# Kernel tuning notes

Hardware: AMD Instinct MI355X
Metric: run time of the kernel (lower is better)

Reference implementation:

```python
import jax, jax.numpy as jnp
import numpy as np

B, N, D, H, FF = 2, 2048, 768, 12, 3072
HD = D // H
RADIUS = 2.0
COORD_DIM = 3
LN_EPS = 1e-5


def _layernorm(x, g, b):
    m = jnp.mean(x, axis=-1, keepdims=True)
    v = jnp.mean((x - m) ** 2, axis=-1, keepdims=True)
    return (x - m) * jax.lax.rsqrt(v + LN_EPS) * g + b


def setup_inputs() -> dict:
    key = jax.random.key(0)
    ks = jax.random.split(key, 16)
    s = 0.02
    return {
        "x": jax.random.normal(ks[0], (B, N, D), jnp.float32),
        "coords": jax.random.uniform(ks[1], (B, N, COORD_DIM), jnp.float32) * 10.0,
        "w_qkv": jax.random.normal(ks[2], (D, 3 * D), jnp.float32) * s,
        "b_qkv": jnp.zeros((3 * D,), jnp.float32),
        "w_out": jax.random.normal(ks[3], (D, D), jnp.float32) * s,
        "b_out": jnp.zeros((D,), jnp.float32),
        "w_ff1": jax.random.normal(ks[4], (D, FF), jnp.float32) * s,
        "b_ff1": jnp.zeros((FF,), jnp.float32),
        "w_ff2": jax.random.normal(ks[5], (FF, D), jnp.float32) * s,
        "b_ff2": jnp.zeros((D,), jnp.float32),
        "g1": jnp.ones((D,), jnp.float32),
        "beta1": jnp.zeros((D,), jnp.float32),
        "g2": jnp.ones((D,), jnp.float32),
        "beta2": jnp.zeros((D,), jnp.float32),
    }


def reference(x, coords, w_qkv, b_qkv, w_out, b_out, w_ff1, b_ff1,
              w_ff2, b_ff2, g1, beta1, g2, beta2):
    # --- attention sub-block ---
    residual = x
    xn = _layernorm(x, g1, beta1)
    qkv = xn @ w_qkv + b_qkv                       # [B,N,3D]
    qkv = qkv.reshape(B, N, 3, H, HD)
    q, k, v = qkv[:, :, 0], qkv[:, :, 1], qkv[:, :, 2]   # [B,N,H,HD]

    # geometric radius mask: attend only to tokens within Euclidean RADIUS
    d2 = jnp.sum((coords[:, :, None, :] - coords[:, None, :, :]) ** 2, axis=-1)  # [B,N,N]
    mask = d2 <= RADIUS * RADIUS                   # self-distance 0 -> always true

    scores = jnp.einsum("bqhd,bkhd->bhqk", q, k) / jnp.sqrt(jnp.float32(HD))
    scores = jnp.where(mask[:, None, :, :], scores, jnp.float32(-1e9))
    attn = jax.nn.softmax(scores, axis=-1)
    attn_out = jnp.einsum("bhqk,bkhd->bqhd", attn, v).reshape(B, N, D)
    attn_out = attn_out @ w_out + b_out            # dropout=0 (eval)
    x = residual + attn_out

    # --- FFN sub-block ---
    residual = x
    xn = _layernorm(x, g2, beta2)
    h = jax.nn.gelu(xn @ w_ff1 + b_ff1, approximate=False)
    ff_out = h @ w_ff2 + b_ff2
    return residual + ff_out
```

## Files before the change

### kernel.cpp

```cpp
#include <hip/hip_runtime.h>
#include <hip/hip_bf16.h>

typedef unsigned short ushort_t;
typedef __attribute__((ext_vector_type(4))) float f32x4;
typedef __attribute__((ext_vector_type(8))) short s16x8;

#define DEV static __device__ __forceinline__

constexpr int Bb = 2, Nn = 2048, Dd = 768, Hh = 12, FFf = 3072;
constexpr int MTOK = Bb * Nn;
constexpr int QKVN = 3 * Dd;

DEV unsigned short f2bf(float f) {
    union { float f; unsigned int i; } x; x.f = f;
    unsigned int r = x.i + 0x7FFFu + ((x.i >> 16) & 1u);
    return (unsigned short)(r >> 16);
}

DEV void gload16(const void* g, void* l) {
    __builtin_amdgcn_global_load_lds(
        (const __attribute__((address_space(1))) void*)g,
        (__attribute__((address_space(3))) void*)l, 16, 0, 0);
}

DEV int xcd_swz(int lin, int n) {
    return (lin & 7) * (n >> 3) + (lin >> 3);
}

DEV float gelu_fast(float x) {
    float u = x * (0.7978845608f + 0.0356774081f * x * x);
    float e = __builtin_amdgcn_exp2f(2.885390082f * u);
    float th = 1.f - 2.f / (e + 1.f);
    return 0.5f * x * (1.f + th);
}

__global__ void k_transpose_all(const float* __restrict__ w_qkv, const float* __restrict__ w_out,
                                const float* __restrict__ w_ff1, const float* __restrict__ w_ff2,
                                unsigned short* __restrict__ o_qkv, unsigned short* __restrict__ o_out,
                                unsigned short* __restrict__ o_ff1, unsigned short* __restrict__ o_ff2) {
    __shared__ float t[32][33];
    int id = blockIdx.x;
    const float* in; unsigned short* out; int K, N, tid;
    if (id < 1728)      { in = w_qkv; out = o_qkv; K = 768;  N = 2304; tid = id; }
    else if (id < 2304) { in = w_out; out = o_out; K = 768;  N = 768;  tid = id - 1728; }
    else if (id < 4608) { in = w_ff1; out = o_ff1; K = 768;  N = 3072; tid = id - 2304; }
    else                { in = w_ff2; out = o_ff2; K = 3072; N = 768;  tid = id - 4608; }
    int nbx = N >> 5;
    int bx = (tid % nbx) * 32, by = (tid / nbx) * 32;
    int tx = threadIdx.x, ty = threadIdx.y;
#pragma unroll
    for (int i = 0; i < 4; i++)
        t[ty + 8 * i][tx] = in[(size_t)(by + ty + 8 * i) * N + bx + tx];
    __syncthreads();
#pragma unroll
    for (int i = 0; i < 4; i++)
        out[(size_t)(bx + ty + 8 * i) * K + by + tx] = f2bf(t[tx][ty + 8 * i]);
}

DEV int cell3(float x, float y, float z) {
    int cx = (int)(x * 0.5f); cx = cx > 4 ? 4 : cx;
    int cy = (int)(y * 0.5f); cy = cy > 4 ? 4 : cy;
    int cz = (int)(z * 0.5f); cz = cz > 4 ? 4 : cz;
    return (cz * 5 + cy) * 5 + cx;
}

__global__ __launch_bounds__(256) void k_sort(const float* __restrict__ coords,
                                              int* __restrict__ s2o,
                                              float4* __restrict__ c4s) {
    int b = blockIdx.y;
    int i = blockIdx.x * 4 + (threadIdx.x >> 6);
    int lane = threadIdx.x & 63;
    const float* cb = coords + (size_t)b * Nn * 3;
    float cix = cb[3 * i], ciy = cb[3 * i + 1], ciz = cb[3 * i + 2];
    int celli = cell3(cix, ciy, ciz);
    int pos = 0;
    for (int it = 0; it < Nn / 64; it++) {
        int j = it * 64 + lane;
        int cj = cell3(cb[3 * j], cb[3 * j + 1], cb[3 * j + 2]);
        bool before = (cj < celli) || (cj == celli && j < i);
        pos += __popcll(__ballot(before));
    }
    if (lane == 0) {
        s2o[b * Nn + pos] = i;
        c4s[b * Nn + pos] = make_float4(cix, ciy, ciz, 0.f);
    }
}

__global__ __launch_bounds__(256) void k_mask(const float4* __restrict__ c4s,
                                              unsigned long long* __restrict__ mb) {
    int qt = blockIdx.x, ks = blockIdx.y, b = blockIdx.z;
    __shared__ float4 ck[256];
    int t = threadIdx.x;
    ck[t] = c4s[b * Nn + ks * 256 + t];
    __syncthreads();
    int r = t >> 2, c = t & 3;
    int q = qt * 64 + r;
    float4 cq = c4s[b * Nn + q];
    unsigned long long w = 0;
#pragma unroll 8
    for (int j = 0; j < 64; j++) {
        float4 k4 = ck[c * 64 + j];
        float dx = __fsub_rn(cq.x, k4.x);
        float dy = __fsub_rn(cq.y, k4.y);
        float dz = __fsub_rn(cq.z, k4.z);
        float d2 = __fadd_rn(__fadd_rn(__fmul_rn(dx, dx), __fmul_rn(dy, dy)),
                             __fmul_rn(dz, dz));
        if (d2 <= 4.0f) w |= 1ull << j;
    }
    mb[((size_t)(b * Nn + q) << 5) + ks * 4 + c] = w;
}

__global__ __launch_bounds__(64) void k_tiles(const unsigned long long* __restrict__ mb,
                                              int* __restrict__ tl) {
    int q64 = blockIdx.x, b = blockIdx.y;
    int lane = threadIdx.x;
    unsigned long long v = 0;
    if (lane < 32) {
        const unsigned long long* base = mb + ((size_t)(b * Nn + q64 * 64) << 5) + lane;
        for (int r = 0; r < 64; r++) v |= base[(size_t)r << 5];
    }
    unsigned long long nz = __ballot(v != 0);
    int idx = __popcll(nz & ((1ull << lane) - 1));
    int* o = tl + (b * 32 + q64) * 33;
    if (v != 0) o[1 + idx] = lane;
    if (lane == 0) o[0] = __popcll(nz);
}

__global__ __launch_bounds__(128) void k_gatherK(const unsigned short* __restrict__ qkv,
                                                 const int* __restrict__ s2o,
                                                 unsigned short* __restrict__ Ksort) {
    int ns = blockIdx.x & (Nn - 1);
    int b = blockIdx.x >> 11;
    int t = threadIdx.x;
    int orig = s2o[b * Nn + ns];
    const s16x8* src = (const s16x8*)(qkv + ((size_t)b * Nn + orig) * QKVN + Dd);
    s16x8* dst = (s16x8*)(Ksort + ((size_t)b * Nn + ns) * Dd);
    if (t < 96) dst[t] = src[t];
}

__global__ __launch_bounds__(256) void k_vt(const unsigned short* __restrict__ qkv,
                                            const int* __restrict__ s2o,
                                            unsigned short* __restrict__ VtT) {
    __shared__ unsigned short Ld[64][72];
    int ns0 = blockIdx.x * 64;
    int bh = blockIdx.y;
    int b = bh / Hh, h = bh % Hh;
    int t = threadIdx.x;
#pragma unroll
    for (int i = 0; i < 2; i++) {
        int item = t + 256 * i;
        int row = item >> 3, ch = (item & 7) * 8;
        int orig = s2o[b * Nn + ns0 + row];
        *(s16x8*)&Ld[row][ch] =
            *(const s16x8*)(qkv + ((size_t)b * Nn + orig) * QKVN + 2 * Dd + h * 64 + ch);
    }
    __syncthreads();
    int vd = (t >> 5) * 8, vkp = (t & 31) * 2;
#pragma unroll
    for (int j = 0; j < 8; j++) {
        unsigned int pack = (unsigned int)Ld[vkp][vd + j] |
                            ((unsigned int)Ld[vkp + 1][vd + j] << 16);
        *(unsigned int*)((char*)VtT +
                         (((size_t)bh * 64 + vd + j) * Nn + ns0 + vkp) * 2) = pack;
    }
}

DEV float wred_sum(float v) {
#pragma unroll
    for (int o = 32; o; o >>= 1) v += __shfl_down(v, o, 64);
    return v;
}

__global__ __launch_bounds__(256) void k_ln(const float* __restrict__ x,
                                            const float* __restrict__ g,
                                            const float* __restrict__ be,
                                            unsigned short* __restrict__ out) {
    int row = blockIdx.x;
    const float* xr = x + (size_t)row * Dd;
    int t = threadIdx.x;
    float v0 = xr[t], v1 = xr[t + 256], v2 = xr[t + 512];
    float s = v0 + v1 + v2;
    float sq = v0 * v0 + v1 * v1 + v2 * v2;
    __shared__ float r1[4], r2[4];
    float ws = wred_sum(s), wq = wred_sum(sq);
    int wid = t >> 6, lane = t & 63;
    if (lane == 0) { r1[wid] = ws; r2[wid] = wq; }
    __syncthreads();
    s = r1[0] + r1[1] + r1[2] + r1[3];
    sq = r2[0] + r2[1] + r2[2] + r2[3];
    float mean = s * (1.f / Dd);
    float var = sq * (1.f / Dd) - mean * mean;
    float rs = rsqrtf(var + 1e-5f);
    unsigned short* orow = out + (size_t)row * Dd;
    orow[t]       = f2bf((v0 - mean) * rs * g[t]       + be[t]);
    orow[t + 256] = f2bf((v1 - mean) * rs * g[t + 256] + be[t + 256]);
    orow[t + 512] = f2bf((v2 - mean) * rs * g[t + 512] + be[t + 512]);
}

#define GEMM_PIPE_LOOP(NT)                                                              \
    stage(0, 0);                                                                        \
    if ((NT) > 1) stage(1, 1);                                                          \
    for (int t = 0; t < (NT); t++) {                                                    \
        int cur = t % 3;                                                                \
        if (t + 2 < (NT)) {                                                             \
            stage((t + 2) % 3, t + 2);                                                  \
            asm volatile("s_waitcnt vmcnt(8)" ::: "memory");                            \
        } else if (t + 1 < (NT)) {                                                      \
            asm volatile("s_waitcnt vmcnt(4)" ::: "memory");                            \
        } else {                                                                        \
            asm volatile("s_waitcnt vmcnt(0)" ::: "memory");                            \
        }                                                                               \
        __builtin_amdgcn_sched_barrier(0);                                              \
        __builtin_amdgcn_s_barrier();                                                   \
        const unsigned short* Ab = As[cur];                                             \
        const unsigned short* Bbp = Bs[cur];                                            \
        s16x8 af[4], bfr[4];                                                            \
        _Pragma("unroll")                                                               \
        for (int i = 0; i < 4; i++) {                                                   \
            af[i]  = *(const s16x8*)&Ab[(wr * 64 + i * 16 + lr) * 32 + lg * 8];         \
            bfr[i] = *(const s16x8*)&Bbp[(wc * 64 + i * 16 + lr) * 32 + lg * 8];        \
        }                                                                               \
        __builtin_amdgcn_s_setprio(1);                                                  \
        _Pragma("unroll")                                                               \
        for (int mi = 0; mi < 4; mi++)                                                  \
            _Pragma("unroll")                                                           \
            for (int ni = 0; ni < 4; ni++)                                              \
                acc[mi][ni] = __builtin_amdgcn_mfma_f32_16x16x32_bf16(                  \
                    af[mi], bfr[ni], acc[mi][ni], 0, 0, 0);                             \
        __builtin_amdgcn_s_setprio(0);                                                  \
        __builtin_amdgcn_s_barrier();                                                   \
    }

template <int EPI>
__global__ __launch_bounds__(256) void k_gemm(const unsigned short* __restrict__ A,
                                              const unsigned short* __restrict__ Bt,
                                              const float* __restrict__ bias,
                                              const float* __restrict__ res,
                                              void* __restrict__ outp,
                                              int M, int N, int K) {
    constexpr int BM = 128, BN = 128, BK = 32;
    __shared__ unsigned short As[3][BM * BK];
    __shared__ unsigned short Bs[3][BN * BK];
    int NB = N >> 7;
    int id = xcd_swz(blockIdx.x, gridDim.x);
    int m0 = (id / NB) * BM, n0 = (id % NB) * BN;
    int t = threadIdx.x;
    int wid = t >> 6, lane = t & 63;
    int wr = wid >> 1, wc = wid & 1;
    int lg = lane >> 4, lr = lane & 15;
    f32x4 acc[4][4] = {};

    int srow = wid * 32 + (lane >> 2);
    int scol = (lane & 3) * 8;
    const unsigned short* Ag = A + (size_t)(m0 + srow) * K + scol;
    const unsigned short* Bg = Bt + (size_t)(n0 + srow) * K + scol;

    auto stage = [&](int buf, int kt) {
        int k0 = kt * BK;
        char* Al = (char*)As[buf] + wid * 2048;
        char* Bl = (char*)Bs[buf] + wid * 2048;
        gload16(Ag + k0, Al);
        gload16(Ag + k0 + (size_t)16 * K, Al + 1024);
        gload16(Bg + k0, Bl);
        gload16(Bg + k0 + (size_t)16 * K, Bl + 1024);
    };
    int nt = K / BK;
    GEMM_PIPE_LOOP(nt)

    int mrow = m0 + wr * 64;
    int ncol = n0 + wc * 64;
#pragma unroll
    for (int mi = 0; mi < 4; mi++) {
#pragma unroll
        for (int ni = 0; ni < 4; ni++) {
            int nn = ncol + ni * 16 + lr;
            float bs = bias[nn];
#pragma unroll
            for (int r = 0; r < 4; r++) {
                int mm = mrow + mi * 16 + lg * 4 + r;
                float v = acc[mi][ni][r] + bs;
                if (EPI == 1) {
                    ((unsigned short*)outp)[(size_t)mm * N + nn] = f2bf(gelu_fast(v));
                } else if (EPI == 2) {
                    v += res[(size_t)mm * N + nn];
                    ((float*)outp)[(size_t)mm * N + nn] = v;
                } else {
                    ((unsigned short*)outp)[(size_t)mm * N + nn] = f2bf(v);
                }
            }
        }
    }
}

template <int SPLIT>
__global__ __launch_bounds__(256) void k_gemm_sk(const unsigned short* __restrict__ A,
                                                 const unsigned short* __restrict__ Bt,
                                                 float* __restrict__ part,
                                                 int M, int N, int K) {
    constexpr int BM = 128, BN = 128, BK = 32;
    __shared__ unsigned short As[3][BM * BK];
    __shared__ unsigned short Bs[3][BN * BK];
    int NB = N >> 7, MB = M >> 7;
    int id = xcd_swz(blockIdx.x, gridDim.x);
    int nb = id % NB;
    int mbk = (id / NB) % MB;
    int kz = id / (NB * MB);
    int m0 = mbk * BM, n0 = nb * BN;
    int Kc = K / SPLIT, kb = kz * (Kc / BK);
    int t = threadIdx.x;
    int wid = t >> 6, lane = t & 63;
    int wr = wid >> 1, wc = wid & 1;
    int lg = lane >> 4, lr = lane & 15;
    f32x4 acc[4][4] = {};

    int srow = wid * 32 + (lane >> 2);
    int scol = (lane & 3) * 8;
    const unsigned short* Ag = A + (size_t)(m0 + srow) * K + scol;
    const unsigned short* Bg = Bt + (size_t)(n0 + srow) * K + scol;

    auto stage = [&](int buf, int kt) {
        int k0 = (kb + kt) * BK;
        char* Al = (char*)As[buf] + wid * 2048;
        char* Bl = (char*)Bs[buf] + wid * 2048;
        gload16(Ag + k0, Al);
        gload16(Ag + k0 + (size_t)16 * K, Al + 1024);
        gload16(Bg + k0, Bl);
        gload16(Bg + k0 + (size_t)16 * K, Bl + 1024);
    };
    int nt = Kc / BK;
    GEMM_PIPE_LOOP(nt)

    float* po = part + (size_t)kz * M * N;
    int mrow = m0 + wr * 64;
    int ncol = n0 + wc * 64;
#pragma unroll
    for (int mi = 0; mi < 4; mi++)
#pragma unroll
        for (int ni = 0; ni < 4; ni++) {
            int nn = ncol + ni * 16 + lr;
#pragma unroll
            for (int r = 0; r < 4; r++) {
                int mm = mrow + mi * 16 + lg * 4 + r;
                po[(size_t)mm * N + nn] = acc[mi][ni][r];
            }
        }
}

__global__ __launch_bounds__(256) void k_reduce2(const float* __restrict__ part,
                                                 const float* __restrict__ bias,
                                                 const float* __restrict__ res,
                                                 float* __restrict__ out,
                                                 int MN, int N) {
    int i = (blockIdx.x * 256 + threadIdx.x) * 4;
    f32x4 a = *(const f32x4*)(part + i);
    f32x4 bq = *(const f32x4*)(part + (size_t)MN + i);
    f32x4 r = *(const f32x4*)(res + i);
    f32x4 bs = *(const f32x4*)(bias + (i % N));
    f32x4 o;
#pragma unroll
    for (int j = 0; j < 4; j++) o[j] = a[j] + bq[j] + bs[j] + r[j];
    *(f32x4*)(out + i) = o;
}

constexpr float SC2 = 0.125f * 1.44269504088896340736f;
constexpr float PMASK = -3.0e38f;
constexpr float MINIT = -1.0e30f;

__global__ __launch_bounds__(256) void k_attn(const unsigned short* __restrict__ qkv,
                                              const unsigned short* __restrict__ Ksort,
                                              const unsigned short* __restrict__ VtT,
                                              const int* __restrict__ s2o,
                                              const uint2* __restrict__ mb,
                                              const int* __restrict__ tl,
                                              unsigned short* __restrict__ out) {
    int lin = blockIdx.x;
    int id = (lin & 7) * 96 + (lin >> 3);
    int q64 = id & 31;
    int hb = id >> 5;
    int h = hb % Hh, b = hb / Hh;
    int bh = b * Hh + h;

    __shared__ __align__(16) char sm[2 * 16384 + 4 * 2048];

    int t = threadIdx.x, wid = t >> 6, lane = t & 63;
    int lg = lane >> 4, lr = lane & 15;
    int sw = lr & 7;
    int qbase = q64 * 64 + wid * 16;

    int oq = s2o[b * Nn + qbase + lr];
    const unsigned short* Qb = qkv + ((size_t)b * Nn + oq) * QKVN + h * 64;
    s16x8 qf0 = *(const s16x8*)(Qb + lg * 8);
    s16x8 qf1 = *(const s16x8*)(Qb + 32 + lg * 8);

    const uint2* mrow = mb + ((size_t)(b * Nn + qbase + lr) << 5);
    const int* tle = tl + (b * 32 + q64) * 33;
    int tlv = (lane < 33) ? tle[lane] : 0;
    int cnt = __shfl(tlv, 0, 64);

    int srow = lane >> 3, sch = lane & 7;
    int krow = wid * 8 + srow;
    int kx = sch ^ (krow & 7);
    const unsigned short* Kg0 = Ksort + ((size_t)b * Nn + krow) * Dd + h * 64 + kx * 8;
    const unsigned short* Vg0 = VtT + ((size_t)bh * 64 + krow) * Nn + kx * 8;
    char* pw = sm + 32768 + wid * 2048 + lr * 128;

    float m2 = MINIT, l_run = 0.f;
    f32x4 oacc[4] = {};

    int tid0 = __shfl(tlv, 1, 64);
    uint2 Mw = mrow[tid0];
    {
        char* Kl = sm + wid * 1024;
        gload16(Kg0 + (size_t)(tid0 * 64) * Dd, Kl);
        gload16(Kg0 + (size_t)(tid0 * 64 + 32) * Dd, Kl + 4096);
        char* Vl = sm + 8192 + wid * 1024;
        gload16(Vg0 + tid0 * 64, Vl);
        gload16(Vg0 + tid0 * 64 + 32 * (size_t)Nn, Vl + 4096);
    }
    __syncthreads();

    for (int ti = 0; ti < cnt; ti++) {
        int cur = ti & 1;
        uint2 MwN;
        if (ti + 1 < cnt) {
            int tidn = __shfl(tlv, 2 + ti, 64);
            char* Kl = sm + (cur ^ 1) * 16384 + wid * 1024;
            gload16(Kg0 + (size_t)(tidn * 64) * Dd, Kl);
            gload16(Kg0 + (size_t)(tidn * 64 + 32) * Dd, Kl + 4096);
            char* Vl = sm + (cur ^ 1) * 16384 + 8192 + wid * 1024;
            gload16(Vg0 + tidn * 64, Vl);
            gload16(Vg0 + tidn * 64 + 32 * (size_t)Nn, Vl + 4096);
            MwN = mrow[tidn];
        }

        if (__any((Mw.x | Mw.y) != 0)) {
            const char* Kbuf = sm + cur * 16384;
            const char* Vbuf = Kbuf + 8192;

            __builtin_amdgcn_s_setprio(1);
            f32x4 st[4];
#pragma unroll
            for (int s = 0; s < 4; s++) {
                const char* kr = Kbuf + (s * 16 + lr) * 128;
                s16x8 kf0 = *(const s16x8*)(kr + ((lg ^ sw) << 4));
                s16x8 kf1 = *(const s16x8*)(kr + (((4 + lg) ^ sw) << 4));
                f32x4 z = {};
                z = __builtin_amdgcn_mfma_f32_16x16x32_bf16(kf0, qf0, z, 0, 0, 0);
                st[s] = __builtin_amdgcn_mfma_f32_16x16x32_bf16(kf1, qf1, z, 0, 0, 0);
            }
            __builtin_amdgcn_s_setprio(0);

            float p[4][4];
            float mt = PMASK;
#pragma unroll
            for (int s = 0; s < 4; s++) {
                unsigned int wsel = (s < 2) ? Mw.x : Mw.y;
#pragma unroll
                for (int r = 0; r < 4; r++) {
                    float sv = st[s][r] * SC2;
                    unsigned int bit = (wsel >> ((s & 1) * 16 + lg * 4 + r)) & 1u;
                    p[s][r] = bit ? sv : PMASK;
                    mt = fmaxf(mt, p[s][r]);
                }
            }
            mt = fmaxf(mt, __shfl_xor(mt, 16, 64));
            mt = fmaxf(mt, __shfl_xor(mt, 32, 64));

            if (!__all(mt <= m2 + 11.5416f)) {
                float mn2 = fmaxf(m2, mt);
                float fac = __builtin_amdgcn_exp2f(m2 - mn2);
                l_run *= fac;
                m2 = mn2;
                float fr[4];
#pragma unroll
                for (int r = 0; r < 4; r++) fr[r] = __shfl(fac, (lane & 48) + lg * 4 + r, 64);
#pragma unroll
                for (int dt = 0; dt < 4; dt++)
#pragma unroll
                    for (int r = 0; r < 4; r++) oacc[dt][r] *= fr[r];
            }

            float lt = 0.f;
#pragma unroll
            for (int s = 0; s < 4; s++)
#pragma unroll
                for (int r = 0; r < 4; r++) {
                    p[s][r] = __builtin_amdgcn_exp2f(p[s][r] - m2);
                    lt += p[s][r];
                }
            lt += __shfl_xor(lt, 16, 64);
            lt += __shfl_xor(lt, 32, 64);
            l_run += lt;

#pragma unroll
            for (int s = 0; s < 4; s++) {
                unsigned int lo = (unsigned int)f2bf(p[s][0]) | ((unsigned int)f2bf(p[s][1]) << 16);
                unsigned int hi = (unsigned int)f2bf(p[s][2]) | ((unsigned int)f2bf(p[s][3]) << 16);
                unsigned long long u = (unsigned long long)lo | ((unsigned long long)hi << 32);
                int chunk = (s * 2 + (lg >> 1)) ^ sw;
                *(unsigned long long*)(pw + (chunk << 4) + (lg & 1) * 8) = u;
            }

            __builtin_amdgcn_s_setprio(1);
#pragma unroll
            for (int c = 0; c < 2; c++) {
                s16x8 pf = *(const s16x8*)(pw + (((c * 4 + lg) ^ sw) << 4));
#pragma unroll
                for (int dt = 0; dt < 4; dt++) {
                    const char* vr = Vbuf + (dt * 16 + lr) * 128;
                    s16x8 vf = *(const s16x8*)(vr + (((c * 4 + lg) ^ sw) << 4));
                    oacc[dt] = __builtin_amdgcn_mfma_f32_16x16x32_bf16(pf, vf, oacc[dt], 0, 0, 0);
                }
            }
            __builtin_amdgcn_s_setprio(0);
        }

        __syncthreads();
        Mw = MwN;
    }

    float lr4[4];
    int orow[4];
#pragma unroll
    for (int r = 0; r < 4; r++) {
        lr4[r] = __shfl(l_run, (lane & 48) + lg * 4 + r, 64);
        orow[r] = s2o[b * Nn + qbase + lg * 4 + r];
    }
#pragma unroll
    for (int dt = 0; dt < 4; dt++)
#pragma unroll
        for (int r = 0; r < 4; r++) {
            float v = oacc[dt][r] / lr4[r];
            out[((size_t)b * Nn + orow[r]) * Dd + h * 64 + dt * 16 + lr] = f2bf(v);
        }
}

extern "C" void kernel_launch(void* const* d_in, const int* in_sizes, int n_in,
                              void* d_out, int out_size, void* d_ws, size_t ws_size,
                              hipStream_t stream) {
    const float* x      = (const float*)d_in[0];
    const float* coords = (const float*)d_in[1];
    const float* w_qkv  = (const float*)d_in[2];
    const float* b_qkv  = (const float*)d_in[3];
    const float* w_out  = (const float*)d_in[4];
    const float* b_out  = (const float*)d_in[5];
    const float* w_ff1  = (const float*)d_in[6];
    const float* b_ff1  = (const float*)d_in[7];
    const float* w_ff2  = (const float*)d_in[8];
    const float* b_ff2  = (const float*)d_in[9];
    const float* g1     = (const float*)d_in[10];
    const float* beta1  = (const float*)d_in[11];
    const float* g2     = (const float*)d_in[12];
    const float* beta2  = (const float*)d_in[13];

    char* ws = (char*)d_ws;
    size_t off = 0;
    auto alloc = [&](size_t bytes) {
        char* p = ws + off;
        off += (bytes + 255) & ~(size_t)255;
        return p;
    };
    unsigned short* w_qkv_t = (unsigned short*)alloc((size_t)QKVN * Dd * 2);
    unsigned short* w_out_t = (unsigned short*)alloc((size_t)Dd * Dd * 2);
    unsigned short* w_ff1_t = (unsigned short*)alloc((size_t)FFf * Dd * 2);
    unsigned short* w_ff2_t = (unsigned short*)alloc((size_t)Dd * FFf * 2);
    float4*         c4s     = (float4*)alloc((size_t)MTOK * 16);
    int*            s2o     = (int*)alloc((size_t)MTOK * 4);
    unsigned long long* mbits = (unsigned long long*)alloc((size_t)MTOK * 32 * 8);
    int*            tl      = (int*)alloc((size_t)Bb * 32 * 33 * 4);
    unsigned short* xn      = (unsigned short*)alloc((size_t)MTOK * Dd * 2);
    unsigned short* hbuf    = (unsigned short*)alloc((size_t)MTOK * FFf * 2);
    float*          x2      = (float*)alloc((size_t)MTOK * Dd * 4);
    unsigned short* attn_o  = (unsigned short*)alloc((size_t)MTOK * Dd * 2);
    unsigned short* qkv     = (unsigned short*)alloc((size_t)MTOK * QKVN * 2);
    unsigned short* Ksort   = (unsigned short*)alloc((size_t)MTOK * Dd * 2);
    unsigned short* VtT     = (unsigned short*)alloc((size_t)Bb * Hh * 64 * Nn * 2);
    float* partial = (float*)qkv;

    k_transpose_all<<<dim3(6912), dim3(32, 8), 0, stream>>>(
        w_qkv, w_out, w_ff1, w_ff2, w_qkv_t, w_out_t, w_ff1_t, w_ff2_t);
    k_sort<<<dim3(Nn / 4, Bb), 256, 0, stream>>>(coords, s2o, c4s);
    k_mask<<<dim3(Nn / 64, 8, Bb), 256, 0, stream>>>(c4s, mbits);
    k_tiles<<<dim3(32, Bb), 64, 0, stream>>>(mbits, tl);

    k_ln<<<MTOK, 256, 0, stream>>>(x, g1, beta1, xn);
    k_gemm<0><<<dim3((QKVN / 128) * (MTOK / 128)), 256, 0, stream>>>(
        xn, w_qkv_t, b_qkv, nullptr, qkv, MTOK, QKVN, Dd);
    k_gatherK<<<dim3(MTOK), 128, 0, stream>>>(qkv, s2o, Ksort);
    k_vt<<<dim3(Nn / 64, Bb * Hh), 256, 0, stream>>>(qkv, s2o, VtT);
    k_attn<<<dim3((Nn / 64) * Hh * Bb), 256, 0, stream>>>(
        qkv, Ksort, VtT, s2o, (const uint2*)mbits, tl, attn_o);
    k_gemm_sk<2><<<dim3((Dd / 128) * (MTOK / 128) * 2), 256, 0, stream>>>(
        attn_o, w_out_t, partial, MTOK, Dd, Dd);
    k_reduce2<<<dim3(MTOK * Dd / 1024), 256, 0, stream>>>(
        partial, b_out, x, x2, MTOK * Dd, Dd);
    k_ln<<<MTOK, 256, 0, stream>>>(x2, g2, beta2, xn);
    k_gemm<1><<<dim3((FFf / 128) * (MTOK / 128)), 256, 0, stream>>>(
        xn, w_ff1_t, b_ff1, nullptr, hbuf, MTOK, FFf, Dd);
    k_gemm_sk<2><<<dim3((Dd / 128) * (MTOK / 128) * 2), 256, 0, stream>>>(
        hbuf, w_ff2_t, partial, MTOK, Dd, FFf);
    k_reduce2<<<dim3(MTOK * Dd / 1024), 256, 0, stream>>>(
        partial, b_ff2, x2, (float*)d_out, MTOK * Dd, Dd);
}
```

Before: 212.4 us.

## Raise split-K to 4, fuse reduce with LayerNorm, drop GEMM setprio

```diff
diff --git a/kernel.cpp b/kernel.cpp
--- a/kernel.cpp
+++ b/kernel.cpp
@@ -220,14 +220,12 @@
             af[i]  = *(const s16x8*)&Ab[(wr * 64 + i * 16 + lr) * 32 + lg * 8];         \
             bfr[i] = *(const s16x8*)&Bbp[(wc * 64 + i * 16 + lr) * 32 + lg * 8];        \
         }                                                                               \
-        __builtin_amdgcn_s_setprio(1);                                                  \
         _Pragma("unroll")                                                               \
         for (int mi = 0; mi < 4; mi++)                                                  \
             _Pragma("unroll")                                                           \
             for (int ni = 0; ni < 4; ni++)                                              \
                 acc[mi][ni] = __builtin_amdgcn_mfma_f32_16x16x32_bf16(                  \
                     af[mi], bfr[ni], acc[mi][ni], 0, 0, 0);                             \
-        __builtin_amdgcn_s_setprio(0);                                                  \
         __builtin_amdgcn_s_barrier();                                                   \
     }
 
@@ -346,19 +344,70 @@
         }
 }
 
-__global__ __launch_bounds__(256) void k_reduce2(const float* __restrict__ part,
+__global__ __launch_bounds__(256) void k_reduce4_ln(const float* __restrict__ part,
+                                                    const float* __restrict__ bias,
+                                                    const float* __restrict__ res,
+                                                    const float* __restrict__ g,
+                                                    const float* __restrict__ be,
+                                                    float* __restrict__ x2,
+                                                    unsigned short* __restrict__ xn,
+                                                    int MN) {
+    int wid = threadIdx.x >> 6, lane = threadIdx.x & 63;
+    int row = blockIdx.x * 4 + wid;
+    size_t base = (size_t)row * Dd;
+    f32x4 v[3];
+    float s = 0.f, sq = 0.f;
+#pragma unroll
+    for (int j = 0; j < 3; j++) {
+        int col = j * 256 + lane * 4;
+        f32x4 a0 = *(const f32x4*)(part + base + col);
+        f32x4 a1 = *(const f32x4*)(part + (size_t)MN + base + col);
+        f32x4 a2 = *(const f32x4*)(part + 2 * (size_t)MN + base + col);
+        f32x4 a3 = *(const f32x4*)(part + 3 * (size_t)MN + base + col);
+        f32x4 r = *(const f32x4*)(res + base + col);
+        f32x4 bs = *(const f32x4*)(bias + col);
+#pragma unroll
+        for (int q = 0; q < 4; q++) {
+            v[j][q] = (a0[q] + a1[q]) + (a2[q] + a3[q]) + bs[q] + r[q];
+            s += v[j][q];
+            sq += v[j][q] * v[j][q];
+        }
+        *(f32x4*)(x2 + base + col) = v[j];
+    }
+    s = wred_sum(s); sq = wred_sum(sq);
+    s = __shfl(s, 0, 64); sq = __shfl(sq, 0, 64);
+    float mean = s * (1.f / Dd);
+    float var = sq * (1.f / Dd) - mean * mean;
+    float rs = rsqrtf(var + 1e-5f);
+#pragma unroll
+    for (int j = 0; j < 3; j++) {
+        int col = j * 256 + lane * 4;
+        f32x4 gg = *(const f32x4*)(g + col);
+        f32x4 bb = *(const f32x4*)(be + col);
+        ushort4 o;
+        o.x = f2bf((v[j][0] - mean) * rs * gg[0] + bb[0]);
+        o.y = f2bf((v[j][1] - mean) * rs * gg[1] + bb[1]);
+        o.z = f2bf((v[j][2] - mean) * rs * gg[2] + bb[2]);
+        o.w = f2bf((v[j][3] - mean) * rs * gg[3] + bb[3]);
+        *(ushort4*)(xn + base + col) = o;
+    }
+}
+
+__global__ __launch_bounds__(256) void k_reduce4(const float* __restrict__ part,
                                                  const float* __restrict__ bias,
                                                  const float* __restrict__ res,
                                                  float* __restrict__ out,
                                                  int MN, int N) {
     int i = (blockIdx.x * 256 + threadIdx.x) * 4;
-    f32x4 a = *(const f32x4*)(part + i);
-    f32x4 bq = *(const f32x4*)(part + (size_t)MN + i);
+    f32x4 a0 = *(const f32x4*)(part + i);
+    f32x4 a1 = *(const f32x4*)(part + (size_t)MN + i);
+    f32x4 a2 = *(const f32x4*)(part + 2 * (size_t)MN + i);
+    f32x4 a3 = *(const f32x4*)(part + 3 * (size_t)MN + i);
     f32x4 r = *(const f32x4*)(res + i);
     f32x4 bs = *(const f32x4*)(bias + (i % N));
     f32x4 o;
 #pragma unroll
-    for (int j = 0; j < 4; j++) o[j] = a[j] + bq[j] + bs[j] + r[j];
+    for (int j = 0; j < 4; j++) o[j] = (a0[j] + a1[j]) + (a2[j] + a3[j]) + bs[j] + r[j];
     *(f32x4*)(out + i) = o;
 }
 
@@ -575,7 +624,7 @@
     unsigned short* qkv     = (unsigned short*)alloc((size_t)MTOK * QKVN * 2);
     unsigned short* Ksort   = (unsigned short*)alloc((size_t)MTOK * Dd * 2);
     unsigned short* VtT     = (unsigned short*)alloc((size_t)Bb * Hh * 64 * Nn * 2);
-    float* partial = (float*)qkv;
+    float*          partial = (float*)alloc((size_t)4 * MTOK * Dd * 4);
 
     k_transpose_all<<<dim3(6912), dim3(32, 8), 0, stream>>>(
         w_qkv, w_out, w_ff1, w_ff2, w_qkv_t, w_out_t, w_ff1_t, w_ff2_t);
@@ -590,15 +639,14 @@
     k_vt<<<dim3(Nn / 64, Bb * Hh), 256, 0, stream>>>(qkv, s2o, VtT);
     k_attn<<<dim3((Nn / 64) * Hh * Bb), 256, 0, stream>>>(
         qkv, Ksort, VtT, s2o, (const uint2*)mbits, tl, attn_o);
-    k_gemm_sk<2><<<dim3((Dd / 128) * (MTOK / 128) * 2), 256, 0, stream>>>(
+    k_gemm_sk<4><<<dim3((Dd / 128) * (MTOK / 128) * 4), 256, 0, stream>>>(
         attn_o, w_out_t, partial, MTOK, Dd, Dd);
-    k_reduce2<<<dim3(MTOK * Dd / 1024), 256, 0, stream>>>(
-        partial, b_out, x, x2, MTOK * Dd, Dd);
-    k_ln<<<MTOK, 256, 0, stream>>>(x2, g2, beta2, xn);
+    k_reduce4_ln<<<dim3(MTOK / 4), 256, 0, stream>>>(
+        partial, b_out, x, g2, beta2, x2, xn, MTOK * Dd);
     k_gemm<1><<<dim3((FFf / 128) * (MTOK / 128)), 256, 0, stream>>>(
         xn, w_ff1_t, b_ff1, nullptr, hbuf, MTOK, FFf, Dd);
-    k_gemm_sk<2><<<dim3((Dd / 128) * (MTOK / 128) * 2), 256, 0, stream>>>(
+    k_gemm_sk<4><<<dim3((Dd / 128) * (MTOK / 128) * 4), 256, 0, stream>>>(
         hbuf, w_ff2_t, partial, MTOK, Dd, FFf);
-    k_reduce2<<<dim3(MTOK * Dd / 1024), 256, 0, stream>>>(
+    k_reduce4<<<dim3(MTOK * Dd / 1024), 256, 0, stream>>>(
         partial, b_ff2, x2, (float*)d_out, MTOK * Dd, Dd);
 }
```

After: 204.3 us. 1.04x faster.
